# Performance work log

Hardware: AMD Instinct MI355X
Metric: run time of the kernel (lower is better)

## Reference

```python
import jax, jax.numpy as jnp
import numpy as np

D, H, FF, E, K, B, S = 1024, 16, 4096, 8, 2, 2, 2048
EPS = 1e-5


def _layernorm(x, g, b):
    mu = x.mean(-1, keepdims=True)
    var = x.var(-1, keepdims=True)
    return (x - mu) * jax.lax.rsqrt(var + EPS) * g + b


def setup_inputs() -> dict:
    key = jax.random.key(0)
    ks = jax.random.split(key, 16)
    s = 0.02
    return {
        "x": jax.random.normal(ks[0], (B, S, D), dtype=jnp.float32),
        "in_proj_w": jax.random.normal(ks[1], (3 * D, D), dtype=jnp.float32) * s,
        "in_proj_b": jnp.zeros((3 * D,), jnp.float32),
        "out_proj_w": jax.random.normal(ks[2], (D, D), dtype=jnp.float32) * s,
        "out_proj_b": jnp.zeros((D,), jnp.float32),
        "ln1_g": jnp.ones((D,), jnp.float32),
        "ln1_b": jnp.zeros((D,), jnp.float32),
        "ln2_g": jnp.ones((D,), jnp.float32),
        "ln2_b": jnp.zeros((D,), jnp.float32),
        "gate_w": jax.random.normal(ks[3], (E, D), dtype=jnp.float32) * s,
        "gate_b": jnp.zeros((E,), jnp.float32),
        "w1": jax.random.normal(ks[4], (E, FF, D), dtype=jnp.float32) * s,
        "b1": jnp.zeros((E, FF), jnp.float32),
        "w2": jax.random.normal(ks[5], (E, D, FF), dtype=jnp.float32) * s,
        "b2": jnp.zeros((E, D), jnp.float32),
    }


def reference(x, in_proj_w, in_proj_b, out_proj_w, out_proj_b,
              ln1_g, ln1_b, ln2_g, ln2_b,
              gate_w, gate_b, w1, b1, w2, b2):
    b, s, d = x.shape
    hd = d // H
    # --- self-attention (pre-LN), dropout = identity (eval) ---
    normed = _layernorm(x, ln1_g, ln1_b)
    qkv = normed @ in_proj_w.T + in_proj_b            # [b,s,3d]
    q, k, v = jnp.split(qkv, 3, axis=-1)
    q = q.reshape(b, s, H, hd).transpose(0, 2, 1, 3)  # [b,h,s,hd]
    k = k.reshape(b, s, H, hd).transpose(0, 2, 1, 3)
    v = v.reshape(b, s, H, hd).transpose(0, 2, 1, 3)
    scores = jnp.einsum('bhqe,bhke->bhqk', q, k) / np.sqrt(hd)
    attn = jax.nn.softmax(scores, axis=-1)
    o = jnp.einsum('bhqk,bhke->bhqe', attn, v)
    o = o.transpose(0, 2, 1, 3).reshape(b, s, d)
    attn_out = o @ out_proj_w.T + out_proj_b
    x = x + attn_out
    present_kv = (normed, normed)
    # --- MoE FFN ---
    n2 = _layernorm(x, ln2_g, ln2_b)
    xf = n2.reshape(-1, d)                             # [T,d]
    T = xf.shape[0]
    logits = xf @ gate_w.T + gate_b                    # [T,E]
    probs = jax.nn.softmax(logits, axis=-1)
    top_v, top_i = jax.lax.top_k(probs, K)             # [T,K]
    top_v = top_v / top_v.sum(-1, keepdims=True)
    # combine weights per (token, expert); topk indices are unique per token
    cw = jnp.zeros((T, E), probs.dtype).at[jnp.arange(T)[:, None], top_i].add(top_v)
    # dense all-experts FFN (mathematically identical to masked gather/scatter)
    h = jnp.einsum('td,efd->etf', xf, w1) + b1[:, None, :]   # [E,T,FF]
    h = jax.nn.gelu(h, approximate=False)
    eo = jnp.einsum('etf,edf->etd', h, w2) + b2[:, None, :]  # [E,T,d]
    moe_out = jnp.einsum('te,etd->td', cw, eo)               # [T,d]
    out = x + moe_out.reshape(b, s, d)
    # --- load balance loss (Switch) ---
    top1 = jnp.argmax(probs, axis=-1)
    f = jnp.mean(jax.nn.one_hot(top1, E, dtype=probs.dtype), axis=0)
    P = probs.mean(axis=0)
    load_loss = 0.01 * E * jnp.sum(f * P)
    return out, load_loss, probs.reshape(b, s, E), present_kv[0]
```

## Files before the change

kernel.cpp:

```cpp
#include <hip/hip_runtime.h>
#include <math.h>

#define D_ 1024
#define H_ 16
#define HD_ 64
#define FF_ 4096
#define E_ 8
#define B_ 2
#define S_ 2048
#define T_ 4096
#define MAXROWS 9216
#define MAXTILES 72

typedef unsigned short u16;
typedef __attribute__((ext_vector_type(4))) float f32x4;
typedef __attribute__((ext_vector_type(8))) __bf16 bf16x8;
typedef __attribute__((ext_vector_type(8))) _Float16 f16x8;
typedef __attribute__((ext_vector_type(4))) unsigned short u16x4;

__device__ __forceinline__ u16 f2bf(float f){
  union { float f; unsigned u; } v; v.f = f;
  unsigned r = v.u + 0x7fffu + ((v.u >> 16) & 1u);
  return (u16)(r >> 16);
}
__device__ __forceinline__ float bf2f(u16 h){
  union { unsigned u; float f; } v; v.u = ((unsigned)h) << 16;
  return v.f;
}
__device__ __forceinline__ void glds16(const void* g, void* l){
  __builtin_amdgcn_global_load_lds((const __attribute__((address_space(1))) void*)g,
                                   (__attribute__((address_space(3))) void*)l, 16, 0, 0);
}
__device__ __forceinline__ bf16x8 ld8(const u16* p){
  return *reinterpret_cast<const bf16x8*>(p);
}
__device__ __forceinline__ f16x8 ldH8(const _Float16* p){
  return *reinterpret_cast<const f16x8*>(p);
}
__device__ __forceinline__ f32x4 mfma16(bf16x8 a, bf16x8 b, f32x4 c){
  return __builtin_amdgcn_mfma_f32_16x16x32_bf16(a, b, c, 0, 0, 0);
}
__device__ __forceinline__ f32x4 mfmaH(f16x8 a, f16x8 b, f32x4 c){
  return __builtin_amdgcn_mfma_f32_16x16x32_f16(a, b, c, 0, 0, 0);
}
__device__ __forceinline__ unsigned pk16(float a, float b){
  auto pk = __builtin_amdgcn_cvt_pkrtz(a, b);
  return __builtin_bit_cast(unsigned, pk);
}

__global__ void __launch_bounds__(256) split_hl_f16_kernel(const float* __restrict__ in,
    _Float16* __restrict__ hi, _Float16* __restrict__ lo, int n4){
  int i = blockIdx.x*blockDim.x + threadIdx.x;
  if (i >= n4) return;
  float4 v = reinterpret_cast<const float4*>(in)[i];
  float vv[4] = {v.x, v.y, v.z, v.w};
  u16x4 h, l;
  #pragma unroll
  for (int j=0;j<4;j++){
    const _Float16 hh = (_Float16)vv[j];
    const _Float16 ll = (_Float16)(vv[j] - (float)hh);
    h[j] = __builtin_bit_cast(u16, hh);
    l[j] = __builtin_bit_cast(u16, ll);
  }
  reinterpret_cast<u16x4*>(hi)[i] = h;
  reinterpret_cast<u16x4*>(lo)[i] = l;
}

__global__ void __launch_bounds__(256) cvt_bf2_kernel(
    const float* __restrict__ in1, u16* __restrict__ out1,
    const float* __restrict__ in2, u16* __restrict__ out2, int n4each){
  int i = blockIdx.x*blockDim.x + threadIdx.x;
  const float* in; u16* out; int j;
  if (i < n4each){ in = in1; out = out1; j = i; }
  else           { in = in2; out = out2; j = i - n4each; }
  float4 v = reinterpret_cast<const float4*>(in)[j];
  u16x4 o;
  o[0]=f2bf(v.x); o[1]=f2bf(v.y); o[2]=f2bf(v.z); o[3]=f2bf(v.w);
  reinterpret_cast<u16x4*>(out)[j] = o;
}

__global__ void __launch_bounds__(256) cvt_f16_kernel(const float* __restrict__ in, _Float16* __restrict__ out, int n4){
  int i = blockIdx.x*blockDim.x + threadIdx.x;
  if (i >= n4) return;
  float4 v = reinterpret_cast<const float4*>(in)[i];
  union { unsigned w[2]; u16x4 u; } o;
  o.w[0] = pk16(v.x, v.y);
  o.w[1] = pk16(v.z, v.w);
  reinterpret_cast<u16x4*>(out)[i] = o.u;
}

template<int OUTMODE, int GATE>
__global__ void __launch_bounds__(256) ln_kernel(const float* __restrict__ x, const float* __restrict__ g,
    const float* __restrict__ bta, float* __restrict__ outf, u16* __restrict__ nout,
    const float* __restrict__ gw, const float* __restrict__ gb,
    float* __restrict__ probs_out, int* __restrict__ top_i, float* __restrict__ cw_w)
{
  const int t = blockIdx.x, tid = threadIdx.x;
  __shared__ float rs[4], rq[4];
  __shared__ float sp[4][E_];
  const float4 v = reinterpret_cast<const float4*>(x + (size_t)t*D_)[tid];
  float s  = v.x+v.y+v.z+v.w;
  float s2 = v.x*v.x+v.y*v.y+v.z*v.z+v.w*v.w;
  #pragma unroll
  for (int o=32;o;o>>=1){ s += __shfl_xor(s,o); s2 += __shfl_xor(s2,o); }
  const int wid=tid>>6, lane=tid&63;
  if (lane==0){ rs[wid]=s; rq[wid]=s2; }
  __syncthreads();
  s  = rs[0]+rs[1]+rs[2]+rs[3];
  s2 = rq[0]+rq[1]+rq[2]+rq[3];
  const float mu  = s*(1.0f/D_);
  const float var = s2*(1.0f/D_) - mu*mu;
  const float inv = rsqrtf(var + 1e-5f);
  const float4 gv = reinterpret_cast<const float4*>(g)[tid];
  const float4 bv = reinterpret_cast<const float4*>(bta)[tid];
  float oo[4];
  oo[0] = (v.x-mu)*inv*gv.x + bv.x;
  oo[1] = (v.y-mu)*inv*gv.y + bv.y;
  oo[2] = (v.z-mu)*inv*gv.z + bv.z;
  oo[3] = (v.w-mu)*inv*gv.w + bv.w;
  const size_t base = (size_t)t*D_ + tid*4;
  if (outf){ outf[base]=oo[0]; outf[base+1]=oo[1]; outf[base+2]=oo[2]; outf[base+3]=oo[3]; }
  if (OUTMODE==1){
    union { unsigned w[2]; u16x4 u; } hv;
    hv.w[0] = pk16(oo[0], oo[1]);
    hv.w[1] = pk16(oo[2], oo[3]);
    reinterpret_cast<u16x4*>(nout)[base>>2] = hv.u;
  } else {
    u16x4 hv;
    hv[0]=f2bf(oo[0]); hv[1]=f2bf(oo[1]); hv[2]=f2bf(oo[2]); hv[3]=f2bf(oo[3]);
    reinterpret_cast<u16x4*>(nout)[base>>2] = hv;
  }
  if (GATE){
    float part[E_];
    #pragma unroll
    for (int e=0;e<E_;e++){
      const float4 wv = reinterpret_cast<const float4*>(gw + (size_t)e*D_)[tid];
      part[e] = oo[0]*wv.x + oo[1]*wv.y + oo[2]*wv.z + oo[3]*wv.w;
    }
    #pragma unroll
    for (int e=0;e<E_;e++){
      #pragma unroll
      for (int o=32;o;o>>=1) part[e] += __shfl_xor(part[e], o);
    }
    if (lane==0){
      #pragma unroll
      for (int e=0;e<E_;e++) sp[wid][e] = part[e];
    }
    __syncthreads();
    if (tid==0){
      float lg[E_], mx=-3e38f;
      #pragma unroll
      for (int e=0;e<E_;e++){
        lg[e] = sp[0][e]+sp[1][e]+sp[2][e]+sp[3][e] + gb[e];
        mx = fmaxf(mx, lg[e]);
      }
      float ex[E_], sm=0.f;
      #pragma unroll
      for (int e=0;e<E_;e++){ ex[e]=__expf(lg[e]-mx); sm+=ex[e]; }
      float p[E_];
      #pragma unroll
      for (int e=0;e<E_;e++){ p[e]=ex[e]/sm; probs_out[(size_t)t*E_+e]=p[e]; }
      int i0=0; float l0=lg[0];
      #pragma unroll
      for (int e=1;e<E_;e++) if (lg[e]>l0){ l0=lg[e]; i0=e; }
      int i1=-1; float l1=-3e38f;
      #pragma unroll
      for (int e=0;e<E_;e++) if (e!=i0 && lg[e]>l1){ l1=lg[e]; i1=e; }
      top_i[2*t]=i0; top_i[2*t+1]=i1;
      const float v0=p[i0], v1=p[i1];
      const float swt=v0+v1;
      cw_w[2*t]=v0/swt; cw_w[2*t+1]=v1/swt;
    }
  }
}

__global__ void __launch_bounds__(256) qkv_kernel(
    const _Float16* __restrict__ A, const _Float16* __restrict__ Bw,
    const float* __restrict__ bias,
    _Float16* __restrict__ qf, _Float16* __restrict__ kf, _Float16* __restrict__ vtf)
{
  __shared__ __align__(16) _Float16 Ash[2][128*32], Bsh[2][128*32];
  const int bid = blockIdx.x, nwg = gridDim.x;
  const int fid = (bid & 7)*(nwg>>3) + (bid>>3);
  const int nt = fid % 24, mt = fid / 24;
  const int tid=threadIdx.x, wid=tid>>6, lane=tid&63;
  const int wr=wid>>1, wc=wid&1;
  const int r16=lane&15, g4=lane>>4;
  const _Float16* Ag = A  + (size_t)mt*128*D_;
  const _Float16* Bg = Bw + (size_t)nt*128*D_;
  const int srow = wid*16 + (lane>>2);
  const int scol = (((lane&3) ^ ((lane>>3)&3)))*8;
  const int sl   = (g4 ^ ((r16>>1)&3))*8;
  f32x4 acc[4][4] = {};
#define QSTAGE(bi, k0) do { \
    _Pragma("unroll") \
    for (int p=0;p<2;p++){ \
      const int r  = p*64 + srow; \
      const int lo = (p*64 + wid*16)*32; \
      glds16(Ag + (size_t)r*D_ + (k0) + scol, &Ash[bi][lo]); \
      glds16(Bg + (size_t)r*D_ + (k0) + scol, &Bsh[bi][lo]); \
    } \
  } while(0)
  QSTAGE(0, 0);
  int cur = 0;
  for (int t=0; t<D_/32; ++t){
    if (t+1 < D_/32){
      QSTAGE(cur^1, (t+1)*32);
      asm volatile("s_waitcnt vmcnt(4)" ::: "memory");
    } else {
      asm volatile("s_waitcnt vmcnt(0)" ::: "memory");
    }
    __syncthreads();
    f16x8 af[4], bfr[4];
    #pragma unroll
    for (int m=0;m<4;m++) af[m]=ldH8(&Ash[cur][(wr*64+m*16+r16)*32 + sl]);
    #pragma unroll
    for (int n=0;n<4;n++) bfr[n]=ldH8(&Bsh[cur][(wc*64+n*16+r16)*32 + sl]);
    #pragma unroll
    for (int m=0;m<4;m++){
      #pragma unroll
      for (int n=0;n<4;n++) acc[m][n] = mfmaH(af[m], bfr[n], acc[m][n]);
    }
    __syncthreads();
    cur ^= 1;
  }
#undef QSTAGE
  #pragma unroll
  for (int m=0;m<4;m++){
    #pragma unroll
    for (int n=0;n<4;n++){
      #pragma unroll
      for (int r=0;r<4;r++){
        const int grow = mt*128 + wr*64 + m*16 + g4*4 + r;
        const int gcol = nt*128 + wc*64 + n*16 + r16;
        const float val = acc[m][n][r] + bias[gcol];
        const int which = gcol>>10, rem = gcol&1023;
        const int hh = rem>>6, ee = rem&63;
        const int bb = grow>>11, ss = grow&2047;
        if (which==0){
          qf[((size_t)(bb*H_+hh)*S_ + ss)*HD_ + ee] = (_Float16)(val * 0.18033688f);
        } else if (which==1){
          kf[((size_t)(bb*H_+hh)*S_ + ss)*HD_ + ee] = (_Float16)val;
        } else {
          const int p32 = 2*(ss & 12) + (ss & 3) + 4*((ss >> 4) & 1);
          const size_t idx = (((size_t)(bb*H_+hh)*(S_/32) + (ss>>5))*HD_ + ee)*32 + p32;
          vtf[idx] = (_Float16)val;
        }
      }
    }
  }
}

__global__ void __launch_bounds__(256) gemm3_kernel(
    const _Float16* __restrict__ A, int lda,
    const _Float16* __restrict__ Bh, const _Float16* __restrict__ Bl, int Kdim,
    const float* __restrict__ bias,
    const float* __restrict__ resid, float* __restrict__ x1out)
{
  __shared__ __align__(16) _Float16 Ash[2][128*32], Bsh[2][128*32], Bsl[2][128*32];
  const int bid = blockIdx.x, nwg = gridDim.x;
  const int fid = (bid & 7)*(nwg>>3) + (bid>>3);
  const int nt = fid & 7, mt = fid >> 3;
  const int tid=threadIdx.x, wid=tid>>6, lane=tid&63;
  const int wr=wid>>1, wc=wid&1;
  const int r16=lane&15, g4=lane>>4;
  const _Float16* Ag  = A  + (size_t)mt*128*lda;
  const _Float16* Bgh = Bh + (size_t)nt*128*Kdim;
  const _Float16* Bgl = Bl + (size_t)nt*128*Kdim;
  const int srow = wid*16 + (lane>>2);
  const int scol = (((lane&3) ^ ((lane>>3)&3)))*8;
  const int sl   = (g4 ^ ((r16>>1)&3))*8;
  f32x4 acc[4][4] = {};
#define G3STAGE(bi, k0) do { \
    _Pragma("unroll") \
    for (int p=0;p<2;p++){ \
      const int r  = p*64 + srow; \
      const int lo = (p*64 + wid*16)*32; \
      glds16(Ag  + (size_t)r*lda  + (k0) + scol, &Ash[bi][lo]); \
      glds16(Bgh + (size_t)r*Kdim + (k0) + scol, &Bsh[bi][lo]); \
      glds16(Bgl + (size_t)r*Kdim + (k0) + scol, &Bsl[bi][lo]); \
    } \
  } while(0)
  G3STAGE(0, 0);
  int cur = 0;
  const int NK = Kdim/32;
  for (int t=0; t<NK; ++t){
    if (t+1 < NK){
      G3STAGE(cur^1, (t+1)*32);
      asm volatile("s_waitcnt vmcnt(6)" ::: "memory");
    } else {
      asm volatile("s_waitcnt vmcnt(0)" ::: "memory");
    }
    __syncthreads();
    f16x8 af[4], bfh[4], bfl[4];
    #pragma unroll
    for (int m=0;m<4;m++){
      const int row = wr*64 + m*16 + r16;
      af[m] = ldH8(&Ash[cur][row*32 + sl]);
    }
    #pragma unroll
    for (int n=0;n<4;n++){
      const int row = wc*64 + n*16 + r16;
      bfh[n] = ldH8(&Bsh[cur][row*32 + sl]);
      bfl[n] = ldH8(&Bsl[cur][row*32 + sl]);
    }
    #pragma unroll
    for (int m=0;m<4;m++){
      #pragma unroll
      for (int n=0;n<4;n++){
        acc[m][n] = mfmaH(af[m], bfl[n], acc[m][n]);
        acc[m][n] = mfmaH(af[m], bfh[n], acc[m][n]);
      }
    }
    __syncthreads();
    cur ^= 1;
  }
#undef G3STAGE
  #pragma unroll
  for (int m=0;m<4;m++){
    #pragma unroll
    for (int n=0;n<4;n++){
      #pragma unroll
      for (int r=0;r<4;r++){
        const int grow = mt*128 + wr*64 + m*16 + g4*4 + r;
        const int gcol = nt*128 + wc*64 + n*16 + r16;
        const float val = acc[m][n][r] + bias[gcol];
        const size_t idx = (size_t)grow*D_ + gcol;
        x1out[idx] = val + resid[idx];
      }
    }
  }
}

__global__ void __launch_bounds__(512, 2) attn10_kernel(
    const _Float16* __restrict__ Qf, const _Float16* __restrict__ Kf,
    const _Float16* __restrict__ Vtf,
    _Float16* __restrict__ Of)
{
  __shared__ __align__(16) _Float16 Kb[2][4096];
  __shared__ __align__(16) _Float16 Vb[2][4096];
  const int bid = blockIdx.x;
  const int wg = (bid & 7) * 64 + (bid >> 3);
  const int bh = wg >> 4, qc = wg & 15;
  const int tid=threadIdx.x, wid=tid>>6, lane=tid&63;
  const int r16=lane&15, g4=lane>>4;
  const int q0 = qc*128 + wid*16;
  const _Float16* Qp = Qf  + (size_t)bh*S_*HD_ + (size_t)(q0+r16)*HD_ + g4*8;
  const _Float16* Kbase = Kf  + (size_t)bh*S_*HD_;
  const _Float16* Vbase = Vtf + (size_t)bh*HD_*S_;
  const f16x8 qf0 = ldH8(Qp);
  const f16x8 qf1 = ldH8(Qp+32);
  f32x4 of[4] = {};
  float m_run = -3e38f, lr = 0.f;

  const int kOff = (wid*8 + (lane>>3))*HD_ + (((lane&7) ^ ((lane>>3)&7)))*8;
  const int vOff = wid*512 + lane*8;
  const int sk0 = (g4 ^ (r16&7))*8;
  const int sk1 = ((g4+4) ^ (r16&7))*8;

#define STAGE(bi, tt) do { \
    glds16(Kbase + (size_t)(tt)*64*HD_ + kOff, (void*)&Kb[bi][wid*512]); \
    glds16(Vbase + (size_t)(tt)*4096   + vOff, (void*)&Vb[bi][wid*512]); \
  } while(0)

#define ATT_HALF(Kh_, Vh_) do { \
    const f16x8 k0v = ldH8((Kh_) + r16*64 + sk0); \
    const f16x8 k1v = ldH8((Kh_) + r16*64 + sk1); \
    const f16x8 k2v = ldH8((Kh_) + (16+r16)*64 + sk0); \
    const f16x8 k3v = ldH8((Kh_) + (16+r16)*64 + sk1); \
    f32x4 sA={}, sB={}; \
    __builtin_amdgcn_s_setprio(1); \
    sA = mfmaH(k0v, qf0, sA); sA = mfmaH(k1v, qf1, sA); \
    sB = mfmaH(k2v, qf0, sB); sB = mfmaH(k3v, qf1, sB); \
    __builtin_amdgcn_s_setprio(0); \
    const float t0=sA[0], t1=sA[1], t2=sA[2], t3=sA[3]; \
    const float t4=sB[0], t5=sB[1], t6=sB[2], t7=sB[3]; \
    const float lmx = fmaxf(fmaxf(fmaxf(t0,t1),fmaxf(t2,t3)), \
                            fmaxf(fmaxf(t4,t5),fmaxf(t6,t7))); \
    if (!__all(lmx <= m_run + 4.0f)) { \
      float mx = fmaxf(lmx, __shfl_xor(lmx,16)); \
      mx = fmaxf(mx, __shfl_xor(mx,32)); \
      const float mn = fmaxf(m_run, mx); \
      const float alp = __builtin_amdgcn_exp2f(m_run - mn); \
      m_run = mn; \
      lr *= alp; \
      const float ao0=__shfl(alp,4*g4), ao1=__shfl(alp,4*g4+1); \
      const float ao2=__shfl(alp,4*g4+2), ao3=__shfl(alp,4*g4+3); \
      _Pragma("unroll") \
      for (int c=0;c<4;c++){ of[c][0]*=ao0; of[c][1]*=ao1; of[c][2]*=ao2; of[c][3]*=ao3; } \
    } \
    const float msh = m_run - 9.0f; \
    const float p0=__builtin_amdgcn_exp2f(t0-msh), p1=__builtin_amdgcn_exp2f(t1-msh); \
    const float p2=__builtin_amdgcn_exp2f(t2-msh), p3=__builtin_amdgcn_exp2f(t3-msh); \
    const float p4=__builtin_amdgcn_exp2f(t4-msh), p5=__builtin_amdgcn_exp2f(t5-msh); \
    const float p6=__builtin_amdgcn_exp2f(t6-msh), p7=__builtin_amdgcn_exp2f(t7-msh); \
    lr += ((p0+p1)+(p2+p3)) + ((p4+p5)+(p6+p7)); \
    union { unsigned w[4]; f16x8 v; } pu; \
    pu.w[0]=pk16(p0,p1); pu.w[1]=pk16(p2,p3); \
    pu.w[2]=pk16(p4,p5); pu.w[3]=pk16(p6,p7); \
    const f16x8 v0v = ldH8((Vh_) + (r16)*32 + g4*8); \
    const f16x8 v1v = ldH8((Vh_) + (16+r16)*32 + g4*8); \
    const f16x8 v2v = ldH8((Vh_) + (32+r16)*32 + g4*8); \
    const f16x8 v3v = ldH8((Vh_) + (48+r16)*32 + g4*8); \
    __builtin_amdgcn_s_setprio(1); \
    of[0] = mfmaH(pu.v, v0v, of[0]); of[1] = mfmaH(pu.v, v1v, of[1]); \
    of[2] = mfmaH(pu.v, v2v, of[2]); of[3] = mfmaH(pu.v, v3v, of[3]); \
    __builtin_amdgcn_s_setprio(0); \
  } while(0)

  STAGE(0, 0);
  int cur = 0;

  for (int t=0; t<32; ++t){
    if (t < 31){
      STAGE(cur^1, t+1);
      asm volatile("s_waitcnt vmcnt(2)" ::: "memory");
    } else {
      asm volatile("s_waitcnt vmcnt(0)" ::: "memory");
    }
    __syncthreads();
    ATT_HALF(&Kb[cur][0],    &Vb[cur][0]);
    ATT_HALF(&Kb[cur][2048], &Vb[cur][2048]);
    __syncthreads();
    cur ^= 1;
  }
#undef ATT_HALF
#undef STAGE

  lr += __shfl_xor(lr,16);
  lr += __shfl_xor(lr,32);
  float li[4];
  #pragma unroll
  for (int r=0;r<4;r++) li[r] = 1.0f / __shfl(lr, 4*g4+r);
  const int bb = bh>>4, hh = bh&15;
  #pragma unroll
  for (int c=0;c<4;c++){
    #pragma unroll
    for (int r=0;r<4;r++){
      const float val = of[c][r] * li[r];
      const int qq = q0 + 4*g4 + r;
      const size_t idx = ((size_t)(bb*S_+qq))*D_ + hh*HD_ + c*16 + r16;
      Of[idx] = (_Float16)val;
    }
  }
}

__global__ void __launch_bounds__(512) scan_kernel(const int* __restrict__ top_i,
    int* __restrict__ goff, int* __restrict__ tile_expert,
    int* __restrict__ assign_token, int* __restrict__ pos_of,
    const float* __restrict__ probs, float* __restrict__ loss_out)
{
  __shared__ int cnt[E_];
  __shared__ int off[E_+1];
  __shared__ float sf[8][E_], sP[8][E_];
  const int tid=threadIdx.x;
  if (tid<E_) cnt[tid]=0;
  __syncthreads();
  for (int t=tid;t<T_;t+=512){
    atomicAdd(&cnt[top_i[2*t]],1);
    atomicAdd(&cnt[top_i[2*t+1]],1);
  }
  __syncthreads();
  if (tid==0){
    off[0]=0;
    for (int e=0;e<E_;e++) off[e+1]=off[e]+((cnt[e]+127)&~127);
    for (int i=0;i<=E_;i++) goff[i]=off[i];
  }
  __syncthreads();
  if (tid<MAXTILES){
    const int r=tid*128; int e=-1;
    for (int j=0;j<E_;j++) if (r>=off[j] && r<off[j+1]) e=j;
    tile_expert[tid]=e;
  }
  const int lane=tid&63;
  const int e=tid>>6;
  int base=off[e];
  for (int c=0;c<T_/64;c++){
    const int t=c*64+lane;
    const int a0=top_i[2*t], a1=top_i[2*t+1];
    const bool f=(a0==e)||(a1==e);
    const unsigned long long m=__ballot(f);
    if (f){
      const int pos = base + (int)__popcll(m & ((1ull<<lane)-1ull));
      assign_token[pos]=t;
      pos_of[2*t + (a0==e?0:1)] = pos;
    }
    base += (int)__popcll(m);
  }
  for (int r=base+lane; r<off[e+1]; r+=64) assign_token[r]=-1;
  __syncthreads();
  for (int r=off[E_]+tid; r<MAXROWS; r+=512) assign_token[r]=-1;
  float fc[E_]={0,0,0,0,0,0,0,0}, Ps[E_]={0,0,0,0,0,0,0,0};
  for (int t=tid;t<T_;t+=512){
    const float* pr = probs + (size_t)t*E_;
    const int a0 = top_i[2*t];
    #pragma unroll
    for (int k=0;k<E_;k++){
      Ps[k] += pr[k];
      fc[k] += (a0==k) ? 1.0f : 0.0f;
    }
  }
  #pragma unroll
  for (int k=0;k<E_;k++){
    #pragma unroll
    for (int o=32;o;o>>=1){ fc[k]+=__shfl_xor(fc[k],o); Ps[k]+=__shfl_xor(Ps[k],o); }
  }
  const int wid8 = tid>>6;
  if (lane==0){
    #pragma unroll
    for (int k=0;k<E_;k++){ sf[wid8][k]=fc[k]; sP[wid8][k]=Ps[k]; }
  }
  __syncthreads();
  if (tid==0){
    float loss=0.f;
    #pragma unroll
    for (int k=0;k<E_;k++){
      float fe=0.f, Pe=0.f;
      #pragma unroll
      for (int w=0;w<8;w++){ fe+=sf[w][k]; Pe+=sP[w][k]; }
      loss += (fe/(float)T_)*(Pe/(float)T_);
    }
    loss_out[0] = 0.01f*(float)E_*loss;
  }
}

template<int MODE>
__global__ void __launch_bounds__(256, 4) gemm_grp_kernel(
    const u16* __restrict__ A, int lda,
    const u16* __restrict__ Bbase, int Kdim, int Nsz, int NT,
    const float* __restrict__ bias,
    const int* __restrict__ tile_expert,
    const int* __restrict__ atok,
    u16* __restrict__ outp)
{
  const int bid = blockIdx.x, nwg = gridDim.x;
  const int fid = (bid & 7)*(nwg>>3) + (bid>>3);
  const int nt = fid % NT, mt = fid / NT;
  const int e = tile_expert[mt];
  if (e<0) return;
  __shared__ __align__(16) u16 Ash[2][128*32], Bsh[2][128*32];
  const int tid=threadIdx.x, wid=tid>>6, lane=tid&63;
  const int wr=wid>>1, wc=wid&1;
  const int r16=lane&15, g4=lane>>4;
  const float* bp = bias + (size_t)e*Nsz;
  const int srow = wid*16 + (lane>>2);
  const int scol = (((lane&3) ^ ((lane>>3)&3)))*8;
  const int sl   = (g4 ^ ((r16>>1)&3))*8;
  const u16* Bg = Bbase + (size_t)e*Nsz*Kdim + (size_t)nt*128*Kdim;
  size_t arow0, arow1;
  if (MODE==2){
    int t0 = atok[mt*128 + srow];      if (t0 < 0) t0 = 0;
    int t1 = atok[mt*128 + 64 + srow]; if (t1 < 0) t1 = 0;
    arow0 = (size_t)t0*lda;
    arow1 = (size_t)t1*lda;
  } else {
    arow0 = (size_t)(mt*128 + srow)*lda;
    arow1 = (size_t)(mt*128 + 64 + srow)*lda;
  }
  f32x4 acc[4][4] = {};
#define GSTAGE(bi, k0) do { \
    glds16(A + arow0 + (k0) + scol, &Ash[bi][(wid*16)*32]); \
    glds16(A + arow1 + (k0) + scol, &Ash[bi][(64 + wid*16)*32]); \
    glds16(Bg + (size_t)(srow)*Kdim      + (k0) + scol, &Bsh[bi][(wid*16)*32]); \
    glds16(Bg + (size_t)(64+srow)*Kdim   + (k0) + scol, &Bsh[bi][(64 + wid*16)*32]); \
  } while(0)
  GSTAGE(0, 0);
  int cur = 0;
  const int NK = Kdim/32;
  for (int t=0; t<NK; ++t){
    if (t+1 < NK){
      GSTAGE(cur^1, (t+1)*32);
      asm volatile("s_waitcnt vmcnt(4)" ::: "memory");
    } else {
      asm volatile("s_waitcnt vmcnt(0)" ::: "memory");
    }
    __syncthreads();
    bf16x8 af[4], bfr[4];
    #pragma unroll
    for (int m=0;m<4;m++) af[m]=ld8(&Ash[cur][(wr*64+m*16+r16)*32 + sl]);
    #pragma unroll
    for (int n=0;n<4;n++) bfr[n]=ld8(&Bsh[cur][(wc*64+n*16+r16)*32 + sl]);
    #pragma unroll
    for (int m=0;m<4;m++){
      #pragma unroll
      for (int n=0;n<4;n++) acc[m][n] = mfma16(af[m], bfr[n], acc[m][n]);
    }
    __syncthreads();
    cur ^= 1;
  }
#undef GSTAGE
  #pragma unroll
  for (int m=0;m<4;m++){
    #pragma unroll
    for (int n=0;n<4;n++){
      #pragma unroll
      for (int r=0;r<4;r++){
        const int grow = mt*128 + wr*64 + m*16 + g4*4 + r;
        const int gcol = nt*128 + wc*64 + n*16 + r16;
        float val = acc[m][n][r] + bp[gcol];
        if (MODE==2){
          const float z = val*(1.0f + 0.044715f*val*val)*2.3021622f;
          val = val / (1.0f + __builtin_amdgcn_exp2f(-z));
        }
        outp[(size_t)grow*Nsz + gcol] = f2bf(val);
      }
    }
  }
}

__global__ void __launch_bounds__(256) combine_kernel(const float* __restrict__ x1,
    const u16* __restrict__ eo, const int* __restrict__ pos_of, const float* __restrict__ cw_w,
    float* __restrict__ out0)
{
  const int t=blockIdx.x, tid=threadIdx.x;
  const int r0=pos_of[2*t], r1=pos_of[2*t+1];
  const float w0=cw_w[2*t], w1=cw_w[2*t+1];
  const u16x4 e0 = reinterpret_cast<const u16x4*>(eo + (size_t)r0*D_)[tid];
  const u16x4 e1 = reinterpret_cast<const u16x4*>(eo + (size_t)r1*D_)[tid];
  const float4 xv = reinterpret_cast<const float4*>(x1 + (size_t)t*D_)[tid];
  float4 o;
  o.x = xv.x + w0*bf2f(e0[0]) + w1*bf2f(e1[0]);
  o.y = xv.y + w0*bf2f(e0[1]) + w1*bf2f(e1[1]);
  o.z = xv.z + w0*bf2f(e0[2]) + w1*bf2f(e1[2]);
  o.w = xv.w + w0*bf2f(e0[3]) + w1*bf2f(e1[3]);
  reinterpret_cast<float4*>(out0 + (size_t)t*D_)[tid] = o;
}

static inline size_t alup(size_t x){ return (x+255)&~(size_t)255; }

extern "C" void kernel_launch(void* const* d_in, const int* in_sizes, int n_in,
                              void* d_out, int out_size, void* d_ws, size_t ws_size,
                              hipStream_t stream) {
  (void)in_sizes; (void)n_in; (void)out_size; (void)ws_size;
  const float* x    = (const float*)d_in[0];
  const float* ipw  = (const float*)d_in[1];
  const float* ipb  = (const float*)d_in[2];
  const float* opw  = (const float*)d_in[3];
  const float* opb  = (const float*)d_in[4];
  const float* ln1g = (const float*)d_in[5];
  const float* ln1b = (const float*)d_in[6];
  const float* ln2g = (const float*)d_in[7];
  const float* ln2b = (const float*)d_in[8];
  const float* gw   = (const float*)d_in[9];
  const float* gb   = (const float*)d_in[10];
  const float* w1   = (const float*)d_in[11];
  const float* b1   = (const float*)d_in[12];
  const float* w2   = (const float*)d_in[13];
  const float* b2   = (const float*)d_in[14];

  float* out0       = (float*)d_out;
  float* loss_out   = out0 + (size_t)T_*D_;
  float* probs_out  = loss_out + 1;
  float* normed_out = probs_out + (size_t)T_*E_;

  char* p = (char*)d_ws;
  auto take = [&](size_t bytes)->void*{ void* r = (void*)p; p += alup(bytes); return r; };

  _Float16* wipf  = (_Float16*)take((size_t)3*D_*D_*2);
  _Float16* wophf = (_Float16*)take((size_t)D_*D_*2);
  _Float16* woplf = (_Float16*)take((size_t)D_*D_*2);
  u16* w1b   = (u16*)take((size_t)E_*FF_*D_*2);
  u16* w2b   = (u16*)take((size_t)E_*D_*FF_*2);
  _Float16* nf16 = (_Float16*)take((size_t)T_*D_*2);
  _Float16* qf  = (_Float16*)take((size_t)T_*D_*2);
  _Float16* kf  = (_Float16*)take((size_t)T_*D_*2);
  _Float16* vtf = (_Float16*)take((size_t)T_*D_*2);
  _Float16* of16 = (_Float16*)take((size_t)T_*D_*2);
  float* x1  = (float*)take((size_t)T_*D_*4);
  u16* n2b   = (u16*)take((size_t)T_*D_*2);
  u16* hbuf  = (u16*)take((size_t)MAXROWS*FF_*2);
  u16* eo    = (u16*)take((size_t)MAXROWS*D_*2);
  int* top_i = (int*)take((size_t)T_*2*4);
  float* cww = (float*)take((size_t)T_*2*4);
  int* posof = (int*)take((size_t)T_*2*4);
  int* goff  = (int*)take((size_t)(E_+1)*4);
  int* texp  = (int*)take((size_t)MAXTILES*4);
  int* atok  = (int*)take((size_t)MAXROWS*4);

  cvt_f16_kernel<<<(3*D_*D_/4+255)/256, 256, 0, stream>>>(ipw, wipf, 3*D_*D_/4);
  split_hl_f16_kernel<<<(D_*D_/4+255)/256, 256, 0, stream>>>(opw, wophf, woplf, D_*D_/4);
  cvt_bf2_kernel<<<(2*(E_*FF_*D_/4)+255)/256, 256, 0, stream>>>(w1, w1b, w2, w2b, E_*FF_*D_/4);

  ln_kernel<1,0><<<T_, 256, 0, stream>>>(x, ln1g, ln1b, normed_out, (u16*)nf16,
                                         nullptr, nullptr, nullptr, nullptr, nullptr);

  qkv_kernel<<<dim3(24*(T_/128)), 256, 0, stream>>>(nf16, wipf, ipb, qf, kf, vtf);

  attn10_kernel<<<B_*H_*(S_/128), 512, 0, stream>>>(qf, kf, vtf, of16);

  gemm3_kernel<<<dim3(8*(T_/128)), 256, 0, stream>>>(
      of16, D_, wophf, woplf, D_, opb, x, x1);

  ln_kernel<2,1><<<T_, 256, 0, stream>>>(x1, ln2g, ln2b, nullptr, n2b,
                                         gw, gb, probs_out, top_i, cww);

  scan_kernel<<<1, 512, 0, stream>>>(top_i, goff, texp, atok, posof, probs_out, loss_out);

  gemm_grp_kernel<2><<<dim3((FF_/128)*MAXTILES), 256, 0, stream>>>(n2b, D_, w1b, D_, FF_, FF_/128, b1, texp, atok, hbuf);
  gemm_grp_kernel<3><<<dim3((D_/128)*MAXTILES), 256, 0, stream>>>(hbuf, FF_, w2b, FF_, D_, D_/128, b2, texp, nullptr, eo);

  combine_kernel<<<T_, 256, 0, stream>>>(x1, eo, posof, cww, out0);
}
```

Baseline: 499.7 us.

## Overlap expert weight bf16 conversion with attention via extra blocks

Merges the in-proj f16 conversion and the out-proj hi/lo split into a single launch. Moves the large w1/w2 fp32-to-bf16 conversion into extra workgroups appended to the attention kernel, so that memory-bound work can overlap with the compute-bound attention blocks. This removes launch overhead and hides conversion bandwidth, at the risk that the converter blocks compete for CUs or delay attention blocks, since they share the kernel's 512-thread launch bounds and LDS allocation.

```diff
diff --git a/kernel.cpp b/kernel.cpp
--- a/kernel.cpp
+++ b/kernel.cpp
@@ -11,6 +11,8 @@
 #define T_ 4096
 #define MAXROWS 9216
 #define MAXTILES 72
+#define ATTNB 512
+#define CVTB 512
 
 typedef unsigned short u16;
 typedef __attribute__((ext_vector_type(4))) float f32x4;
@@ -48,45 +50,33 @@
   return __builtin_bit_cast(unsigned, pk);
 }
 
-__global__ void __launch_bounds__(256) split_hl_f16_kernel(const float* __restrict__ in,
-    _Float16* __restrict__ hi, _Float16* __restrict__ lo, int n4){
+__global__ void __launch_bounds__(256) cvt_wproj_kernel(
+    const float* __restrict__ ipw, _Float16* __restrict__ wipf,
+    const float* __restrict__ opw, _Float16* __restrict__ woph, _Float16* __restrict__ wopl,
+    int n4a, int n4b)
+{
   int i = blockIdx.x*blockDim.x + threadIdx.x;
-  if (i >= n4) return;
-  float4 v = reinterpret_cast<const float4*>(in)[i];
-  float vv[4] = {v.x, v.y, v.z, v.w};
-  u16x4 h, l;
-  #pragma unroll
-  for (int j=0;j<4;j++){
-    const _Float16 hh = (_Float16)vv[j];
-    const _Float16 ll = (_Float16)(vv[j] - (float)hh);
-    h[j] = __builtin_bit_cast(u16, hh);
-    l[j] = __builtin_bit_cast(u16, ll);
-  }
-  reinterpret_cast<u16x4*>(hi)[i] = h;
-  reinterpret_cast<u16x4*>(lo)[i] = l;
-}
-
-__global__ void __launch_bounds__(256) cvt_bf2_kernel(
-    const float* __restrict__ in1, u16* __restrict__ out1,
-    const float* __restrict__ in2, u16* __restrict__ out2, int n4each){
-  int i = blockIdx.x*blockDim.x + threadIdx.x;
-  const float* in; u16* out; int j;
-  if (i < n4each){ in = in1; out = out1; j = i; }
-  else           { in = in2; out = out2; j = i - n4each; }
-  float4 v = reinterpret_cast<const float4*>(in)[j];
-  u16x4 o;
-  o[0]=f2bf(v.x); o[1]=f2bf(v.y); o[2]=f2bf(v.z); o[3]=f2bf(v.w);
-  reinterpret_cast<u16x4*>(out)[j] = o;
-}
-
-__global__ void __launch_bounds__(256) cvt_f16_kernel(const float* __restrict__ in, _Float16* __restrict__ out, int n4){
-  int i = blockIdx.x*blockDim.x + threadIdx.x;
-  if (i >= n4) return;
-  float4 v = reinterpret_cast<const float4*>(in)[i];
-  union { unsigned w[2]; u16x4 u; } o;
-  o.w[0] = pk16(v.x, v.y);
-  o.w[1] = pk16(v.z, v.w);
-  reinterpret_cast<u16x4*>(out)[i] = o.u;
+  if (i < n4a){
+    float4 v = reinterpret_cast<const float4*>(ipw)[i];
+    union { unsigned w[2]; u16x4 u; } o;
+    o.w[0] = pk16(v.x, v.y);
+    o.w[1] = pk16(v.z, v.w);
+    reinterpret_cast<u16x4*>(wipf)[i] = o.u;
+  } else if (i < n4a + n4b){
+    const int j = i - n4a;
+    float4 v = reinterpret_cast<const float4*>(opw)[j];
+    float vv[4] = {v.x, v.y, v.z, v.w};
+    u16x4 h, l;
+    #pragma unroll
+    for (int k=0;k<4;k++){
+      const _Float16 hh = (_Float16)vv[k];
+      const _Float16 ll = (_Float16)(vv[k] - (float)hh);
+      h[k] = __builtin_bit_cast(u16, hh);
+      l[k] = __builtin_bit_cast(u16, ll);
+    }
+    reinterpret_cast<u16x4*>(woph)[j] = h;
+    reinterpret_cast<u16x4*>(wopl)[j] = l;
+  }
 }
 
 template<int OUTMODE, int GATE>
@@ -332,14 +322,29 @@
   }
 }
 
-__global__ void __launch_bounds__(512, 2) attn10_kernel(
+__global__ void __launch_bounds__(512, 2) attn_cvt_kernel(
     const _Float16* __restrict__ Qf, const _Float16* __restrict__ Kf,
-    const _Float16* __restrict__ Vtf,
-    _Float16* __restrict__ Of)
+    const _Float16* __restrict__ Vtf, _Float16* __restrict__ Of,
+    const float* __restrict__ w1, u16* __restrict__ w1b,
+    const float* __restrict__ w2, u16* __restrict__ w2b, int n4each)
 {
+  const int bid = blockIdx.x;
+  if (bid >= ATTNB){
+    const int cb = bid - ATTNB;
+    const size_t stride = (size_t)CVTB*512;
+    for (size_t i = (size_t)cb*512 + threadIdx.x; i < (size_t)2*n4each; i += stride){
+      const float* in; u16* out; size_t j;
+      if (i < (size_t)n4each){ in = w1; out = w1b; j = i; }
+      else                    { in = w2; out = w2b; j = i - n4each; }
+      float4 v = reinterpret_cast<const float4*>(in)[j];
+      u16x4 o;
+      o[0]=f2bf(v.x); o[1]=f2bf(v.y); o[2]=f2bf(v.z); o[3]=f2bf(v.w);
+      reinterpret_cast<u16x4*>(out)[j] = o;
+    }
+    return;
+  }
   __shared__ __align__(16) _Float16 Kb[2][4096];
   __shared__ __align__(16) _Float16 Vb[2][4096];
-  const int bid = blockIdx.x;
   const int wg = (bid & 7) * 64 + (bid >> 3);
   const int bh = wg >> 4, qc = wg & 15;
   const int tid=threadIdx.x, wid=tid>>6, lane=tid&63;
@@ -677,16 +682,16 @@
   int* texp  = (int*)take((size_t)MAXTILES*4);
   int* atok  = (int*)take((size_t)MAXROWS*4);
 
-  cvt_f16_kernel<<<(3*D_*D_/4+255)/256, 256, 0, stream>>>(ipw, wipf, 3*D_*D_/4);
-  split_hl_f16_kernel<<<(D_*D_/4+255)/256, 256, 0, stream>>>(opw, wophf, woplf, D_*D_/4);
-  cvt_bf2_kernel<<<(2*(E_*FF_*D_/4)+255)/256, 256, 0, stream>>>(w1, w1b, w2, w2b, E_*FF_*D_/4);
+  cvt_wproj_kernel<<<(3*D_*D_/4 + D_*D_/4 + 255)/256, 256, 0, stream>>>(
+      ipw, wipf, opw, wophf, woplf, 3*D_*D_/4, D_*D_/4);
 
   ln_kernel<1,0><<<T_, 256, 0, stream>>>(x, ln1g, ln1b, normed_out, (u16*)nf16,
                                          nullptr, nullptr, nullptr, nullptr, nullptr);
 
   qkv_kernel<<<dim3(24*(T_/128)), 256, 0, stream>>>(nf16, wipf, ipb, qf, kf, vtf);
 
-  attn10_kernel<<<B_*H_*(S_/128), 512, 0, stream>>>(qf, kf, vtf, of16);
+  attn_cvt_kernel<<<ATTNB + CVTB, 512, 0, stream>>>(qf, kf, vtf, of16,
+                                                    w1, w1b, w2, w2b, E_*FF_*D_/4);
 
   gemm3_kernel<<<dim3(8*(T_/128)), 256, 0, stream>>>(
       of16, D_, wophf, woplf, D_, opb, x, x1);
```

After: 494.2 us (median of 3 runs). About the same (-1.1%).
